# Performance work log

Hardware: AMD Instinct MI355X
Metric: run time of the kernel (lower is better)

## Reference

```python
import jax, jax.numpy as jnp
import numpy as np

LN_EPS = 1e-5

def _next_fast_len(n):
    # smallest 5-smooth integer >= n (matches scipy.fftpack.next_fast_len)
    while True:
        m = n
        for p in (2, 3, 5):
            while m % p == 0:
                m //= p
        if m == 1:
            return n
        n += 1

def _conv1d_fft(x, w):
    # x: (b, h, N, d), convolved along axis -2 against w: (h, M) along axis -1.
    # Matches the torch reference: multiply by conj(rfft(w)), roll by -1, take last N.
    N = x.shape[-2]
    M = w.shape[-1]
    L = _next_fast_len(N + M - 1)
    fx = jnp.fft.rfft(x, n=L, axis=-2)                    # (b, h, F, d) complex
    fw = jnp.fft.rfft(w, n=L, axis=-1)                    # (h, F) complex
    out = jnp.fft.irfft(fx * jnp.conj(fw)[..., None], L, axis=-2)
    out = jnp.roll(out, -1, axis=-2)
    return out[..., L - N:, :]                            # (b, h, N, d)

def setup_inputs() -> dict:
    key = jax.random.key(0)
    ks = jax.random.split(key, 5)
    b, n, d, h = 4, 4096, 1024, 8
    dh = d // h
    s = 0.02
    return {
        "x": jax.random.normal(ks[0], (b, n, d), jnp.float32),
        "ln_gamma": jnp.ones((d,), jnp.float32),
        "ln_beta": jnp.zeros((d,), jnp.float32),
        "w_in": jax.random.normal(ks[1], (d, d), jnp.float32) * s,
        "b_in": jnp.zeros((d,), jnp.float32),
        "initial_state": jax.random.normal(ks[2], (h, dh), jnp.float32),
        "alpha": jax.random.normal(ks[3], (h,), jnp.float32),
        "w_out": jax.random.normal(ks[4], (d, d), jnp.float32) * s,
        "b_out": jnp.zeros((d,), jnp.float32),
    }

def reference(x, ln_gamma, ln_beta, w_in, b_in, initial_state, alpha, w_out, b_out):
    b, n, d = x.shape
    h, dh = initial_state.shape
    # LayerNorm
    mu = jnp.mean(x, axis=-1, keepdims=True)
    var = jnp.mean((x - mu) ** 2, axis=-1, keepdims=True)
    xn = (x - mu) * jax.lax.rsqrt(var + LN_EPS) * ln_gamma + ln_beta
    # project_in (torch Linear: y = x @ W.T + b)
    xp = xn @ w_in.T + b_in
    # b n (h d) -> b h n d
    xh = xp.reshape(b, n, h, dh).transpose(0, 2, 1, 3)
    # prepend learned initial state, then first difference along n
    init = jnp.broadcast_to(initial_state[None, :, None, :], (b, h, 1, dh))
    xc = jnp.concatenate([init, xh], axis=2)
    xd = xc[:, :, 1:] - xc[:, :, :-1]                     # (b, h, n, dh)
    # EMA weights per head
    a = jax.nn.sigmoid(alpha)[:, None]                    # (h, 1)
    ar = jnp.arange(n)
    w = a * (1.0 - a) ** ar[::-1]                         # (h, n)
    out = _conv1d_fft(xd, w)
    # initial-state contribution
    init_w = (1.0 - a) ** (ar + 1)                        # (h, n)
    out = out + init_w[:, :, None] * initial_state[:, None, :]
    # b h n d -> b n (h d), then project_out
    out = out.transpose(0, 2, 1, 3).reshape(b, n, d)
    return out @ w_out.T + b_out
```

## Files before the change

### kernel.cpp

```cpp
#include <hip/hip_runtime.h>
#include <stdint.h>

typedef float  f32x4 __attribute__((ext_vector_type(4)));
typedef __bf16 bf16x8 __attribute__((ext_vector_type(8)));
typedef short  s16x8 __attribute__((ext_vector_type(8)));
typedef unsigned short u16;

static __device__ __forceinline__ u16 f2bf(float f) {
  unsigned u = __float_as_uint(f);
  u += 0x7fffu + ((u >> 16) & 1u);
  return (u16)(u >> 16);
}
static __device__ __forceinline__ float bf2f(u16 u) {
  return __uint_as_float(((unsigned)u) << 16);
}

static __device__ __forceinline__ void async_copy16(void* lds, const void* g) {
  __builtin_amdgcn_global_load_lds(
      (const __attribute__((address_space(1))) unsigned int*)g,
      (__attribute__((address_space(3))) unsigned int*)lds, 16, 0, 0);
}

__global__ __launch_bounds__(256) void cvt2_k(const float* __restrict__ in0,
                                              const float* __restrict__ in1,
                                              u16* __restrict__ out0,
                                              u16* __restrict__ out1, int n4) {
  int i = blockIdx.x * 256 + threadIdx.x;
  const float* in = (i < n4) ? in0 : in1;
  u16* out = (i < n4) ? out0 : out1;
  int idx = (i < n4) ? i : i - n4;
  float4 v = reinterpret_cast<const float4*>(in)[idx];
  ushort4 o;
  o.x = f2bf(v.x); o.y = f2bf(v.y); o.z = f2bf(v.z); o.w = f2bf(v.w);
  reinterpret_cast<ushort4*>(out)[idx] = o;
}

__global__ __launch_bounds__(256) void ln_k(const float* __restrict__ x,
                                            const float* __restrict__ g,
                                            const float* __restrict__ b,
                                            u16* __restrict__ xn) {
  const int D = 1024;
  const int row = blockIdx.x;
  const int tid = threadIdx.x;
  const float4 v = reinterpret_cast<const float4*>(x + (size_t)row * D)[tid];
  float s  = v.x + v.y + v.z + v.w;
  float s2 = v.x * v.x + v.y * v.y + v.z * v.z + v.w * v.w;
  #pragma unroll
  for (int off = 32; off > 0; off >>= 1) {
    s  += __shfl_down(s, off);
    s2 += __shfl_down(s2, off);
  }
  __shared__ float red[8];
  const int lane = tid & 63, wv = tid >> 6;
  if (lane == 0) { red[wv] = s; red[4 + wv] = s2; }
  __syncthreads();
  s  = red[0] + red[1] + red[2] + red[3];
  s2 = red[4] + red[5] + red[6] + red[7];
  const float mu   = s * (1.0f / D);
  const float var  = s2 * (1.0f / D) - mu * mu;
  const float rstd = rsqrtf(var + 1e-5f);
  const float4 gv = reinterpret_cast<const float4*>(g)[tid];
  const float4 bv = reinterpret_cast<const float4*>(b)[tid];
  ushort4 o;
  o.x = f2bf((v.x - mu) * rstd * gv.x + bv.x);
  o.y = f2bf((v.y - mu) * rstd * gv.y + bv.y);
  o.z = f2bf((v.z - mu) * rstd * gv.z + bv.z);
  o.w = f2bf((v.w - mu) * rstd * gv.w + bv.w);
  reinterpret_cast<ushort4*>(xn + (size_t)row * D)[tid] = o;
}

template<int MODE>
__global__ __launch_bounds__(256) void gemm_bt_k(const u16* __restrict__ A,
                                                 const u16* __restrict__ Bm,
                                                 const float* __restrict__ bias,
                                                 void* __restrict__ Cv,
                                                 const float* __restrict__ alpha,
                                                 float* __restrict__ Lp,
                                                 int M, int N, int K) {
  const int tid  = threadIdx.x;
  const int lane = tid & 63;
  const int wv   = tid >> 6;
  const int ntN  = N >> 7;
  const int nwg  = (M >> 7) * ntN;
  const int bid  = blockIdx.x;
  const int wgid = (bid & 7) * (nwg >> 3) + (bid >> 3);
  const int mt = wgid / ntN, nt = wgid % ntN;
  const int m0 = mt << 7, n0 = nt << 7;

  __shared__ __align__(16) u16 smem[32768];
  __shared__ float sRed[128];

  const int trow = tid >> 3;
  const int tch  = tid & 7;
  const int csw  = (tch ^ (trow & 7)) << 3;
  const u16* gA = A  + (size_t)(m0 + trow) * K + csw;
  const u16* gB = Bm + (size_t)(n0 + trow) * K + csw;
  const int lofs = trow * 64 + (tch << 3);

  f32x4 acc[4][4];
  #pragma unroll
  for (int i = 0; i < 4; ++i)
    #pragma unroll
    for (int j = 0; j < 4; ++j) acc[i][j] = f32x4{0.f, 0.f, 0.f, 0.f};

  const int wr  = (wv >> 1) << 6;
  const int wc  = (wv & 1) << 6;
  const int fr  = lane & 15;
  const int fkc = lane >> 4;
  const int sx  = fr & 7;

  const int nk = K >> 6;
  int buf = 0;

  #pragma unroll
  for (int r = 0; r < 4; ++r) {
    async_copy16(&smem[lofs + r * 2048], gA + (size_t)r * 32 * K);
    async_copy16(&smem[16384 + lofs + r * 2048], gB + (size_t)r * 32 * K);
  }
  __syncthreads();

  for (int t = 0; t < nk; ++t) {
    if (t + 1 < nk) {
      const size_t ko = (size_t)(t + 1) << 6;
      const int nb = (buf ^ 1) * 8192;
      #pragma unroll
      for (int r = 0; r < 4; ++r) {
        async_copy16(&smem[nb + lofs + r * 2048], gA + ko + (size_t)r * 32 * K);
        async_copy16(&smem[16384 + nb + lofs + r * 2048], gB + ko + (size_t)r * 32 * K);
      }
    }
    const u16* bA = smem + buf * 8192;
    const u16* bB = smem + 16384 + buf * 8192;
    #pragma unroll
    for (int s = 0; s < 2; ++s) {
      const int ch = ((((s << 2) + fkc) ^ sx) << 3);
      s16x8 af[4], bfr[4];
      #pragma unroll
      for (int i = 0; i < 4; ++i)
        af[i] = *reinterpret_cast<const s16x8*>(&bA[(wr + i * 16 + fr) * 64 + ch]);
      #pragma unroll
      for (int j = 0; j < 4; ++j)
        bfr[j] = *reinterpret_cast<const s16x8*>(&bB[(wc + j * 16 + fr) * 64 + ch]);
      #pragma unroll
      for (int i = 0; i < 4; ++i)
        #pragma unroll
        for (int j = 0; j < 4; ++j)
          acc[i][j] = __builtin_amdgcn_mfma_f32_16x16x32_bf16(
              __builtin_bit_cast(bf16x8, af[i]),
              __builtin_bit_cast(bf16x8, bfr[j]), acc[i][j], 0, 0, 0);
    }
    __syncthreads();
    buf ^= 1;
  }

  float* sC = (float*)smem;
  const int cr = (lane >> 4) << 2;
  const int cc = lane & 15;
  float bv[4];
  #pragma unroll
  for (int nj = 0; nj < 4; ++nj) bv[nj] = bias[n0 + wc + nj * 16 + cc];
  #pragma unroll
  for (int mi = 0; mi < 4; ++mi)
    #pragma unroll
    for (int nj = 0; nj < 4; ++nj)
      #pragma unroll
      for (int rr = 0; rr < 4; ++rr) {
        const int row = wr + mi * 16 + cr + rr;
        const int col = wc + nj * 16 + cc;
        sC[row * 128 + (col ^ ((row & 4) << 2))] = acc[mi][nj][rr] + bv[nj];
      }
  __syncthreads();
  #pragma unroll 4
  for (int it = 0; it < 16; ++it) {
    const int row  = it * 8 + (tid >> 5);
    const int col0 = (tid & 31) * 4;
    f32x4 v = *(const f32x4*)&sC[row * 128 + (col0 ^ ((row & 4) << 2))];
    const size_t goff = (size_t)(m0 + row) * N + n0 + col0;
    if (MODE == 1) {
      ushort4 o; o.x = f2bf(v[0]); o.y = f2bf(v[1]); o.z = f2bf(v[2]); o.w = f2bf(v[3]);
      *(ushort4*)&((u16*)Cv)[goff] = o;
    } else {
      *(f32x4*)&((float*)Cv)[goff] = v;
    }
  }
  if (MODE == 1) {
    const int col = tid & 127;
    const int hh = (n0 + col) >> 7;
    const float a  = 1.0f / (1.0f + __expf(-alpha[hh]));
    const float rw = 1.0f - a;
    float r64 = rw;
    #pragma unroll
    for (int s = 0; s < 6; ++s) r64 *= r64;
    const bool lo = (tid < 128);
    const int rbase  = lo ? 1 : 64;
    const int nsteps = lo ? 63 : 64;
    float prev = sC[(rbase - 1) * 128 + (col ^ (((rbase - 1) & 4) << 2))];
    float L = 0.f;
    #pragma unroll 8
    for (int t = rbase; t < rbase + 64; ++t) {
      if (t - rbase >= nsteps) break;
      const float w = sC[t * 128 + (col ^ ((t & 4) << 2))];
      L = rw * L + a * (w - prev);
      prev = w;
    }
    if (!lo) sRed[col] = L;
    __syncthreads();
    if (lo) {
      const float Lt = r64 * L + sRed[col];
      const int bb = m0 >> 12;
      const int q  = (m0 >> 7) & 31;
      Lp[((size_t)bb * 32 + q) * 1024 + n0 + col] = Lt;
    }
  }
}

__global__ __launch_bounds__(256) void ema_carry_k(const u16* __restrict__ xpb,
                                                   const float* __restrict__ alpha,
                                                   const float* __restrict__ init,
                                                   float* __restrict__ carry) {
  const int Dd = 1024, nCh = 32;
  const int idx = blockIdx.x * 256 + threadIdx.x;
  const int c  = idx & (Dd - 1);
  const int bb = idx >> 10;
  const int h = c >> 7;
  const float a = 1.0f / (1.0f + __expf(-alpha[h]));
  const float r = 1.0f - a;
  float q_ = r, r127 = 1.0f;
  #pragma unroll
  for (int s = 0; s < 7; ++s) { r127 *= q_; q_ *= q_; }
  const float rT = r127 * r;
  float cin = init[c];
  float prevv = cin;
  for (int q = 0; q < nCh; ++q) {
    const size_t rowb = (size_t)bb * 4096 + (size_t)q * 128;
    const float v0 = bf2f(xpb[rowb * Dd + c]);
    const size_t off = ((size_t)bb * nCh + q) * Dd + c;
    const float L = carry[off] + a * r127 * (v0 - prevv);
    carry[off] = cin;
    cin = rT * cin + L;
    prevv = bf2f(xpb[(rowb + 127) * Dd + c]);
  }
}

__global__ __launch_bounds__(256) void ema_apply_k(const u16* __restrict__ xp,
                                                   const float* __restrict__ alpha,
                                                   const float* __restrict__ init,
                                                   const float* __restrict__ carry,
                                                   u16* __restrict__ ob) {
  const int Nn = 4096, Dd = 1024, T = 128, nCh = 32;
  int bid = blockIdx.x;
  const int cg = bid & 1;  bid >>= 1;
  const int q  = bid & 31; bid >>= 5;
  const int bb = bid;
  const int c = cg * 512 + threadIdx.x * 2;
  const int h = c >> 7;
  const float a = 1.0f / (1.0f + __expf(-alpha[h]));
  const float r = 1.0f - a;
  const u16* px = xp + ((size_t)bb * Nn + (size_t)q * T) * Dd + c;
  u16* po = ob + ((size_t)bb * Nn + (size_t)q * T) * Dd + c;
  float2 Oin = *(const float2*)(carry + ((size_t)bb * nCh + q) * Dd + c);
  float O0 = Oin.x, O1 = Oin.y;
  float p0, p1;
  if (q == 0) { p0 = init[c]; p1 = init[c + 1]; }
  else { ushort2 pv = *(const ushort2*)(px - Dd); p0 = bf2f(pv.x); p1 = bf2f(pv.y); }
  #pragma unroll 4
  for (int t = 0; t < T; ++t) {
    ushort2 v = *(const ushort2*)(px + (size_t)t * Dd);
    float v0 = bf2f(v.x), v1 = bf2f(v.y);
    O0 = r * O0 + a * (v0 - p0);
    O1 = r * O1 + a * (v1 - p1);
    p0 = v0; p1 = v1;
    ushort2 o; o.x = f2bf(O0); o.y = f2bf(O1);
    *(ushort2*)(po + (size_t)t * Dd) = o;
  }
}

extern "C" void kernel_launch(void* const* d_in, const int* in_sizes, int n_in,
                              void* d_out, int out_size, void* d_ws, size_t ws_size,
                              hipStream_t stream) {
  const float* x     = (const float*)d_in[0];
  const float* ln_g  = (const float*)d_in[1];
  const float* ln_b  = (const float*)d_in[2];
  const float* w_in  = (const float*)d_in[3];
  const float* b_in  = (const float*)d_in[4];
  const float* init  = (const float*)d_in[5];
  const float* alpha = (const float*)d_in[6];
  const float* w_out = (const float*)d_in[7];
  const float* b_out = (const float*)d_in[8];
  float* out = (float*)d_out;

  const int B = 4, N = 4096, D = 1024;
  const int M = B * N;

  char* p = (char*)d_ws;
  u16*   xn  = (u16*)p; p += (size_t)M * D * sizeof(u16);
  u16*   wi  = (u16*)p; p += (size_t)D * D * sizeof(u16);
  u16*   wo  = (u16*)p; p += (size_t)D * D * sizeof(u16);
  u16*   xpb = (u16*)p; p += (size_t)M * D * sizeof(u16);
  float* cr  = (float*)p; p += (size_t)B * 32 * D * sizeof(float);
  u16*   ob  = (u16*)p;

  const int n4 = D * D / 4;
  cvt2_k<<<dim3(2 * n4 / 256), dim3(256), 0, stream>>>(w_in, w_out, wi, wo, n4);
  ln_k<<<dim3(M), dim3(256), 0, stream>>>(x, ln_g, ln_b, xn);
  gemm_bt_k<1><<<dim3((M / 128) * (D / 128)), dim3(256), 0, stream>>>(
      xn, wi, b_in, xpb, alpha, cr, M, D, D);
  ema_carry_k<<<dim3(B * D / 256), dim3(256), 0, stream>>>(xpb, alpha, init, cr);
  ema_apply_k<<<dim3(B * 32 * 2), dim3(256), 0, stream>>>(xpb, alpha, init, cr, ob);
  gemm_bt_k<0><<<dim3((M / 128) * (D / 128)), dim3(256), 0, stream>>>(
      ob, wo, b_out, out, nullptr, nullptr, M, D, D);
}
```

Measured before the change: 143.8 us.

## Enlarge GEMM tiles to 256x256 with 512-thread workgroups

Both projection GEMMs now use 256x256 output tiles computed by eight waves, each holding an 8x4 grid of MFMA accumulators, instead of 128x128 tiles on four waves. The epilogue writes the tile in two 128-row halves through LDS, and the fused EMA partial-sum logic is adapted to emit one carry per half. This raises operand reuse per LDS load and halves global traffic per FLOP. In exchange it uses 128KB of LDS per block, more registers, and only 256 workgroups, which may limit occupancy and load balance across CUs.

```diff
diff --git a/kernel.cpp b/kernel.cpp
--- a/kernel.cpp
+++ b/kernel.cpp
@@ -70,79 +70,80 @@
 }
 
 template<int MODE>
-__global__ __launch_bounds__(256) void gemm_bt_k(const u16* __restrict__ A,
-                                                 const u16* __restrict__ Bm,
-                                                 const float* __restrict__ bias,
-                                                 void* __restrict__ Cv,
-                                                 const float* __restrict__ alpha,
-                                                 float* __restrict__ Lp,
-                                                 int M, int N, int K) {
+__global__ __launch_bounds__(512, 2) void gemm_bt_k(const u16* __restrict__ A,
+                                                    const u16* __restrict__ Bm,
+                                                    const float* __restrict__ bias,
+                                                    void* __restrict__ Cv,
+                                                    const float* __restrict__ alpha,
+                                                    float* __restrict__ Lp,
+                                                    int M, int N, int K) {
   const int tid  = threadIdx.x;
   const int lane = tid & 63;
   const int wv   = tid >> 6;
-  const int ntN  = N >> 7;
-  const int nwg  = (M >> 7) * ntN;
+  const int wrr  = wv >> 2;
+  const int wcc  = wv & 3;
+  const int ntN  = N >> 8;
+  const int nwg  = (M >> 8) * ntN;
   const int bid  = blockIdx.x;
   const int wgid = (bid & 7) * (nwg >> 3) + (bid >> 3);
   const int mt = wgid / ntN, nt = wgid % ntN;
-  const int m0 = mt << 7, n0 = nt << 7;
-
-  __shared__ __align__(16) u16 smem[32768];
-  __shared__ float sRed[128];
-
-  const int trow = tid >> 3;
-  const int tch  = tid & 7;
-  const int csw  = (tch ^ (trow & 7)) << 3;
-  const u16* gA = A  + (size_t)(m0 + trow) * K + csw;
-  const u16* gB = Bm + (size_t)(n0 + trow) * K + csw;
-  const int lofs = trow * 64 + (tch << 3);
-
-  f32x4 acc[4][4];
-  #pragma unroll
-  for (int i = 0; i < 4; ++i)
+  const int m0 = mt << 8, n0 = nt << 8;
+
+  __shared__ __align__(16) u16 smem[65536];
+  __shared__ float sRed[256];
+
+  const int u   = tid >> 3;
+  const int tch = tid & 7;
+  const int csw = (tch ^ (u & 7)) << 3;
+  const int lofs = u * 64 + (tch << 3);
+  const u16* gA = A  + (size_t)(m0 + u) * K + csw;
+  const u16* gB = Bm + (size_t)(n0 + u) * K + csw;
+
+  f32x4 acc[8][4];
+  #pragma unroll
+  for (int i = 0; i < 8; ++i)
     #pragma unroll
     for (int j = 0; j < 4; ++j) acc[i][j] = f32x4{0.f, 0.f, 0.f, 0.f};
 
-  const int wr  = (wv >> 1) << 6;
-  const int wc  = (wv & 1) << 6;
   const int fr  = lane & 15;
   const int fkc = lane >> 4;
   const int sx  = fr & 7;
-
-  const int nk = K >> 6;
+  const int nk  = K >> 6;
   int buf = 0;
 
   #pragma unroll
   for (int r = 0; r < 4; ++r) {
-    async_copy16(&smem[lofs + r * 2048], gA + (size_t)r * 32 * K);
-    async_copy16(&smem[16384 + lofs + r * 2048], gB + (size_t)r * 32 * K);
+    async_copy16(&smem[lofs + r * 4096], gA + (size_t)(r * 64) * K);
+    async_copy16(&smem[32768 + lofs + r * 4096], gB + (size_t)(r * 64) * K);
   }
   __syncthreads();
 
   for (int t = 0; t < nk; ++t) {
     if (t + 1 < nk) {
       const size_t ko = (size_t)(t + 1) << 6;
-      const int nb = (buf ^ 1) * 8192;
+      const int nb = (buf ^ 1) * 16384;
       #pragma unroll
       for (int r = 0; r < 4; ++r) {
-        async_copy16(&smem[nb + lofs + r * 2048], gA + ko + (size_t)r * 32 * K);
-        async_copy16(&smem[16384 + nb + lofs + r * 2048], gB + ko + (size_t)r * 32 * K);
+        async_copy16(&smem[nb + lofs + r * 4096], gA + ko + (size_t)(r * 64) * K);
+        async_copy16(&smem[32768 + nb + lofs + r * 4096], gB + ko + (size_t)(r * 64) * K);
       }
     }
-    const u16* bA = smem + buf * 8192;
-    const u16* bB = smem + 16384 + buf * 8192;
+    const u16* bA = smem + buf * 16384;
+    const u16* bB = smem + 32768 + buf * 16384;
     #pragma unroll
     for (int s = 0; s < 2; ++s) {
       const int ch = ((((s << 2) + fkc) ^ sx) << 3);
-      s16x8 af[4], bfr[4];
-      #pragma unroll
-      for (int i = 0; i < 4; ++i)
-        af[i] = *reinterpret_cast<const s16x8*>(&bA[(wr + i * 16 + fr) * 64 + ch]);
+      s16x8 af[8], bfr[4];
+      #pragma unroll
+      for (int i = 0; i < 8; ++i)
+        af[i] = *reinterpret_cast<const s16x8*>(
+            &bA[(wrr * 128 + i * 16 + fr) * 64 + ch]);
       #pragma unroll
       for (int j = 0; j < 4; ++j)
-        bfr[j] = *reinterpret_cast<const s16x8*>(&bB[(wc + j * 16 + fr) * 64 + ch]);
-      #pragma unroll
-      for (int i = 0; i < 4; ++i)
+        bfr[j] = *reinterpret_cast<const s16x8*>(
+            &bB[(wcc * 64 + j * 16 + fr) * 64 + ch]);
+      #pragma unroll
+      for (int i = 0; i < 8; ++i)
         #pragma unroll
         for (int j = 0; j < 4; ++j)
           acc[i][j] = __builtin_amdgcn_mfma_f32_16x16x32_bf16(
@@ -158,58 +159,65 @@
   const int cc = lane & 15;
   float bv[4];
   #pragma unroll
-  for (int nj = 0; nj < 4; ++nj) bv[nj] = bias[n0 + wc + nj * 16 + cc];
-  #pragma unroll
-  for (int mi = 0; mi < 4; ++mi)
-    #pragma unroll
-    for (int nj = 0; nj < 4; ++nj)
-      #pragma unroll
-      for (int rr = 0; rr < 4; ++rr) {
-        const int row = wr + mi * 16 + cr + rr;
-        const int col = wc + nj * 16 + cc;
-        sC[row * 128 + (col ^ ((row & 4) << 2))] = acc[mi][nj][rr] + bv[nj];
+  for (int nj = 0; nj < 4; ++nj) bv[nj] = bias[n0 + wcc * 64 + nj * 16 + cc];
+
+  #pragma unroll
+  for (int p = 0; p < 2; ++p) {
+    __syncthreads();
+    if (wrr == p) {
+      #pragma unroll
+      for (int mi = 0; mi < 8; ++mi)
+        #pragma unroll
+        for (int nj = 0; nj < 4; ++nj)
+          #pragma unroll
+          for (int rr = 0; rr < 4; ++rr) {
+            const int row = mi * 16 + cr + rr;
+            const int col = wcc * 64 + nj * 16 + cc;
+            sC[row * 256 + (col ^ ((row & 4) << 2))] = acc[mi][nj][rr] + bv[nj];
+          }
+    }
+    __syncthreads();
+    #pragma unroll 4
+    for (int it = 0; it < 16; ++it) {
+      const int row  = it * 8 + (tid >> 6);
+      const int col0 = (tid & 63) * 4;
+      f32x4 v = *(const f32x4*)&sC[row * 256 + (col0 ^ ((row & 4) << 2))];
+      const size_t goff = (size_t)(m0 + p * 128 + row) * N + n0 + col0;
+      if (MODE == 1) {
+        ushort4 o; o.x = f2bf(v[0]); o.y = f2bf(v[1]); o.z = f2bf(v[2]); o.w = f2bf(v[3]);
+        *(ushort4*)&((u16*)Cv)[goff] = o;
+      } else {
+        *(f32x4*)&((float*)Cv)[goff] = v;
       }
-  __syncthreads();
-  #pragma unroll 4
-  for (int it = 0; it < 16; ++it) {
-    const int row  = it * 8 + (tid >> 5);
-    const int col0 = (tid & 31) * 4;
-    f32x4 v = *(const f32x4*)&sC[row * 128 + (col0 ^ ((row & 4) << 2))];
-    const size_t goff = (size_t)(m0 + row) * N + n0 + col0;
+    }
     if (MODE == 1) {
-      ushort4 o; o.x = f2bf(v[0]); o.y = f2bf(v[1]); o.z = f2bf(v[2]); o.w = f2bf(v[3]);
-      *(ushort4*)&((u16*)Cv)[goff] = o;
-    } else {
-      *(f32x4*)&((float*)Cv)[goff] = v;
-    }
-  }
-  if (MODE == 1) {
-    const int col = tid & 127;
-    const int hh = (n0 + col) >> 7;
-    const float a  = 1.0f / (1.0f + __expf(-alpha[hh]));
-    const float rw = 1.0f - a;
-    float r64 = rw;
-    #pragma unroll
-    for (int s = 0; s < 6; ++s) r64 *= r64;
-    const bool lo = (tid < 128);
-    const int rbase  = lo ? 1 : 64;
-    const int nsteps = lo ? 63 : 64;
-    float prev = sC[(rbase - 1) * 128 + (col ^ (((rbase - 1) & 4) << 2))];
-    float L = 0.f;
-    #pragma unroll 8
-    for (int t = rbase; t < rbase + 64; ++t) {
-      if (t - rbase >= nsteps) break;
-      const float w = sC[t * 128 + (col ^ ((t & 4) << 2))];
-      L = rw * L + a * (w - prev);
-      prev = w;
-    }
-    if (!lo) sRed[col] = L;
-    __syncthreads();
-    if (lo) {
-      const float Lt = r64 * L + sRed[col];
-      const int bb = m0 >> 12;
-      const int q  = (m0 >> 7) & 31;
-      Lp[((size_t)bb * 32 + q) * 1024 + n0 + col] = Lt;
+      const int col = tid & 255;
+      const int hh = (n0 + col) >> 7;
+      const float a  = 1.0f / (1.0f + __expf(-alpha[hh]));
+      const float rw = 1.0f - a;
+      float r64 = rw;
+      #pragma unroll
+      for (int s = 0; s < 6; ++s) r64 *= r64;
+      const bool lo = (tid < 256);
+      const int rbase  = lo ? 1 : 64;
+      const int nsteps = lo ? 63 : 64;
+      float prev = sC[(rbase - 1) * 256 + (col ^ (((rbase - 1) & 4) << 2))];
+      float L = 0.f;
+      #pragma unroll 8
+      for (int t = rbase; t < rbase + 64; ++t) {
+        if (t - rbase >= nsteps) break;
+        const float w = sC[t * 256 + (col ^ ((t & 4) << 2))];
+        L = rw * L + a * (w - prev);
+        prev = w;
+      }
+      if (!lo) sRed[col] = L;
+      __syncthreads();
+      if (lo) {
+        const float Lt = r64 * L + sRed[col];
+        const int bb = m0 >> 12;
+        const int q  = ((m0 >> 7) & 31) + p;
+        Lp[((size_t)bb * 32 + q) * 1024 + n0 + col] = Lt;
+      }
     }
   }
 }
@@ -303,10 +311,10 @@
   const int n4 = D * D / 4;
   cvt2_k<<<dim3(2 * n4 / 256), dim3(256), 0, stream>>>(w_in, w_out, wi, wo, n4);
   ln_k<<<dim3(M), dim3(256), 0, stream>>>(x, ln_g, ln_b, xn);
-  gemm_bt_k<1><<<dim3((M / 128) * (D / 128)), dim3(256), 0, stream>>>(
+  gemm_bt_k<1><<<dim3((M / 256) * (D / 256)), dim3(512), 0, stream>>>(
       xn, wi, b_in, xpb, alpha, cr, M, D, D);
   ema_carry_k<<<dim3(B * D / 256), dim3(256), 0, stream>>>(xpb, alpha, init, cr);
   ema_apply_k<<<dim3(B * 32 * 2), dim3(256), 0, stream>>>(xpb, alpha, init, cr, ob);
-  gemm_bt_k<0><<<dim3((M / 128) * (D / 128)), dim3(256), 0, stream>>>(
+  gemm_bt_k<0><<<dim3((M / 256) * (D / 256)), dim3(512), 0, stream>>>(
       ob, wo, b_out, out, nullptr, nullptr, M, D, D);
 }
```

Measured after the change: 138.8 us. 1.04x faster.

## Halve GEMM LDS footprint with BK=32 tiles and two-pass epilogue

Applied to the files above, without the earlier changes.

The GEMM's K-step shrinks from 64 to 32, which halves the staged A/B tiles and LDS use (32 KB instead of 64 KB+). The epilogue now writes the C tile through LDS in two 64-row halves, so it fits the smaller buffer. The per-column EMA partial scan is folded into those passes and run sequentially by 128 threads, which drops the split scan and its sRed reduction. The goal is more resident workgroups per CU. The cost is twice as many barriers per K loop, less MFMA work per barrier, and a serial 128-step EMA loop on half the threads.

```diff
diff --git a/kernel.cpp b/kernel.cpp
--- a/kernel.cpp
+++ b/kernel.cpp
@@ -87,15 +87,15 @@
   const int mt = wgid / ntN, nt = wgid % ntN;
   const int m0 = mt << 7, n0 = nt << 7;
 
-  __shared__ __align__(16) u16 smem[32768];
-  __shared__ float sRed[128];
-
-  const int trow = tid >> 3;
-  const int tch  = tid & 7;
-  const int csw  = (tch ^ (trow & 7)) << 3;
-  const u16* gA = A  + (size_t)(m0 + trow) * K + csw;
-  const u16* gB = Bm + (size_t)(n0 + trow) * K + csw;
-  const int lofs = trow * 64 + (tch << 3);
+  __shared__ __align__(16) u16 smem[16384];
+
+  const int ro  = tid >> 2;
+  const int tc  = tid & 3;
+  const u16* gA0 = A  + (size_t)(m0 + ro) * K + ((tc ^ (ro & 3)) << 3);
+  const u16* gA1 = A  + (size_t)(m0 + 64 + ro) * K + ((tc ^ ((64 + ro) & 3)) << 3);
+  const u16* gB0 = Bm + (size_t)(n0 + ro) * K + ((tc ^ (ro & 3)) << 3);
+  const u16* gB1 = Bm + (size_t)(n0 + 64 + ro) * K + ((tc ^ ((64 + ro) & 3)) << 3);
+  const int lofs = ro * 32 + (tc << 3);
 
   f32x4 acc[4][4];
   #pragma unroll
@@ -107,48 +107,46 @@
   const int wc  = (wv & 1) << 6;
   const int fr  = lane & 15;
   const int fkc = lane >> 4;
-  const int sx  = fr & 7;
-
-  const int nk = K >> 6;
+  const int nk  = K >> 5;
   int buf = 0;
 
-  #pragma unroll
-  for (int r = 0; r < 4; ++r) {
-    async_copy16(&smem[lofs + r * 2048], gA + (size_t)r * 32 * K);
-    async_copy16(&smem[16384 + lofs + r * 2048], gB + (size_t)r * 32 * K);
-  }
+  async_copy16(&smem[lofs],         gA0);
+  async_copy16(&smem[2048 + lofs],  gA1);
+  async_copy16(&smem[8192 + lofs],  gB0);
+  async_copy16(&smem[10240 + lofs], gB1);
   __syncthreads();
 
   for (int t = 0; t < nk; ++t) {
     if (t + 1 < nk) {
-      const size_t ko = (size_t)(t + 1) << 6;
-      const int nb = (buf ^ 1) * 8192;
-      #pragma unroll
-      for (int r = 0; r < 4; ++r) {
-        async_copy16(&smem[nb + lofs + r * 2048], gA + ko + (size_t)r * 32 * K);
-        async_copy16(&smem[16384 + nb + lofs + r * 2048], gB + ko + (size_t)r * 32 * K);
-      }
-    }
-    const u16* bA = smem + buf * 8192;
-    const u16* bB = smem + 16384 + buf * 8192;
+      const size_t ko = (size_t)(t + 1) << 5;
+      const int nb = (buf ^ 1) * 4096;
+      async_copy16(&smem[nb + lofs],         gA0 + ko);
+      async_copy16(&smem[nb + 2048 + lofs],  gA1 + ko);
+      async_copy16(&smem[8192 + nb + lofs],  gB0 + ko);
+      async_copy16(&smem[8192 + nb + 2048 + lofs], gB1 + ko);
+    }
+    const u16* bA = smem + buf * 4096;
+    const u16* bB = smem + 8192 + buf * 4096;
+    s16x8 af[4], bfr[4];
     #pragma unroll
-    for (int s = 0; s < 2; ++s) {
-      const int ch = ((((s << 2) + fkc) ^ sx) << 3);
-      s16x8 af[4], bfr[4];
-      #pragma unroll
-      for (int i = 0; i < 4; ++i)
-        af[i] = *reinterpret_cast<const s16x8*>(&bA[(wr + i * 16 + fr) * 64 + ch]);
+    for (int i = 0; i < 4; ++i) {
+      const int row = wr + i * 16 + fr;
+      af[i] = *reinterpret_cast<const s16x8*>(
+          &bA[row * 32 + ((fkc ^ (row & 3)) << 3)]);
+    }
+    #pragma unroll
+    for (int j = 0; j < 4; ++j) {
+      const int row = wc + j * 16 + fr;
+      bfr[j] = *reinterpret_cast<const s16x8*>(
+          &bB[row * 32 + ((fkc ^ (row & 3)) << 3)]);
+    }
+    #pragma unroll
+    for (int i = 0; i < 4; ++i)
       #pragma unroll
       for (int j = 0; j < 4; ++j)
-        bfr[j] = *reinterpret_cast<const s16x8*>(&bB[(wc + j * 16 + fr) * 64 + ch]);
-      #pragma unroll
-      for (int i = 0; i < 4; ++i)
-        #pragma unroll
-        for (int j = 0; j < 4; ++j)
-          acc[i][j] = __builtin_amdgcn_mfma_f32_16x16x32_bf16(
-              __builtin_bit_cast(bf16x8, af[i]),
-              __builtin_bit_cast(bf16x8, bfr[j]), acc[i][j], 0, 0, 0);
-    }
+        acc[i][j] = __builtin_amdgcn_mfma_f32_16x16x32_bf16(
+            __builtin_bit_cast(bf16x8, af[i]),
+            __builtin_bit_cast(bf16x8, bfr[j]), acc[i][j], 0, 0, 0);
     __syncthreads();
     buf ^= 1;
   }
@@ -159,58 +157,58 @@
   float bv[4];
   #pragma unroll
   for (int nj = 0; nj < 4; ++nj) bv[nj] = bias[n0 + wc + nj * 16 + cc];
-  #pragma unroll
-  for (int mi = 0; mi < 4; ++mi)
-    #pragma unroll
-    for (int nj = 0; nj < 4; ++nj)
+
+  float emaL = 0.f, emaPrev = 0.f, a_ = 0.f, rw_ = 0.f;
+  const int ecol = tid & 127;
+  if (MODE == 1) {
+    const int hh = (n0 + ecol) >> 7;
+    a_  = 1.0f / (1.0f + __expf(-alpha[hh]));
+    rw_ = 1.0f - a_;
+  }
+
+  #pragma unroll
+  for (int p = 0; p < 2; ++p) {
+    __syncthreads();
+    if ((wv >> 1) == p) {
       #pragma unroll
-      for (int rr = 0; rr < 4; ++rr) {
-        const int row = wr + mi * 16 + cr + rr;
-        const int col = wc + nj * 16 + cc;
-        sC[row * 128 + (col ^ ((row & 4) << 2))] = acc[mi][nj][rr] + bv[nj];
+      for (int mi = 0; mi < 4; ++mi)
+        #pragma unroll
+        for (int nj = 0; nj < 4; ++nj)
+          #pragma unroll
+          for (int rr = 0; rr < 4; ++rr) {
+            const int lrow = mi * 16 + cr + rr;
+            const int col  = wc + nj * 16 + cc;
+            sC[lrow * 128 + (col ^ ((lrow & 4) << 2))] = acc[mi][nj][rr] + bv[nj];
+          }
+    }
+    __syncthreads();
+    #pragma unroll 4
+    for (int it = 0; it < 8; ++it) {
+      const int lrow = it * 8 + (tid >> 5);
+      const int col0 = (tid & 31) * 4;
+      f32x4 v = *(const f32x4*)&sC[lrow * 128 + (col0 ^ ((lrow & 4) << 2))];
+      const size_t goff = (size_t)(m0 + p * 64 + lrow) * N + n0 + col0;
+      if (MODE == 1) {
+        ushort4 o; o.x = f2bf(v[0]); o.y = f2bf(v[1]); o.z = f2bf(v[2]); o.w = f2bf(v[3]);
+        *(ushort4*)&((u16*)Cv)[goff] = o;
+      } else {
+        *(f32x4*)&((float*)Cv)[goff] = v;
       }
-  __syncthreads();
-  #pragma unroll 4
-  for (int it = 0; it < 16; ++it) {
-    const int row  = it * 8 + (tid >> 5);
-    const int col0 = (tid & 31) * 4;
-    f32x4 v = *(const f32x4*)&sC[row * 128 + (col0 ^ ((row & 4) << 2))];
-    const size_t goff = (size_t)(m0 + row) * N + n0 + col0;
-    if (MODE == 1) {
-      ushort4 o; o.x = f2bf(v[0]); o.y = f2bf(v[1]); o.z = f2bf(v[2]); o.w = f2bf(v[3]);
-      *(ushort4*)&((u16*)Cv)[goff] = o;
-    } else {
-      *(f32x4*)&((float*)Cv)[goff] = v;
-    }
-  }
-  if (MODE == 1) {
-    const int col = tid & 127;
-    const int hh = (n0 + col) >> 7;
-    const float a  = 1.0f / (1.0f + __expf(-alpha[hh]));
-    const float rw = 1.0f - a;
-    float r64 = rw;
-    #pragma unroll
-    for (int s = 0; s < 6; ++s) r64 *= r64;
-    const bool lo = (tid < 128);
-    const int rbase  = lo ? 1 : 64;
-    const int nsteps = lo ? 63 : 64;
-    float prev = sC[(rbase - 1) * 128 + (col ^ (((rbase - 1) & 4) << 2))];
-    float L = 0.f;
-    #pragma unroll 8
-    for (int t = rbase; t < rbase + 64; ++t) {
-      if (t - rbase >= nsteps) break;
-      const float w = sC[t * 128 + (col ^ ((t & 4) << 2))];
-      L = rw * L + a * (w - prev);
-      prev = w;
-    }
-    if (!lo) sRed[col] = L;
-    __syncthreads();
-    if (lo) {
-      const float Lt = r64 * L + sRed[col];
-      const int bb = m0 >> 12;
-      const int q  = (m0 >> 7) & 31;
-      Lp[((size_t)bb * 32 + q) * 1024 + n0 + col] = Lt;
-    }
+    }
+    if (MODE == 1 && tid < 128) {
+      int lr = (p == 0) ? 1 : 0;
+      if (p == 0) emaPrev = sC[ecol];
+      for (; lr < 64; ++lr) {
+        const float w = sC[lr * 128 + (ecol ^ ((lr & 4) << 2))];
+        emaL = rw_ * emaL + a_ * (w - emaPrev);
+        emaPrev = w;
+      }
+    }
+  }
+  if (MODE == 1 && tid < 128) {
+    const int bb = m0 >> 12;
+    const int q  = (m0 >> 7) & 31;
+    Lp[((size_t)bb * 32 + q) * 1024 + n0 + ecol] = emaL;
   }
 }
 
```

Result: slower. 158.7 us (+10.4%).
